# Optimization experiments

Hardware: AMD Instinct MI355X
Metric: run time of the kernel (lower is better)

Reference implementation:

```python
import jax, jax.numpy as jnp
import numpy as np

N = 1_048_576   # sampled points
E = 32          # grid feature dim (static_grid.out_dim / xyzt_grid.out_dim)
H = 64          # hidden_dim
GEO = 15        # geo_feat_dim
V = 3           # input_ch_views


def setup_inputs() -> dict:
    key = jax.random.key(0)
    ks = jax.random.split(key, 32)
    rn = lambda k, s: jax.random.normal(k, s, jnp.float32)
    w = lambda k, i, o: rn(k, (i, o)) * (1.0 / np.sqrt(i))
    inp = {
        'embedded_xyz': rn(ks[0], (N, E)),
        'embedded_xyzt': rn(ks[1], (N, E)),
        'embedded_xyzt_cam': rn(ks[2], (N, E)),
        'input_views': rn(ks[3], (N, V)),
        'keep_mask_bg': (jax.random.uniform(ks[4], (N,)) < 0.95).astype(jnp.float32),
        'keep_mask_fg': (jax.random.uniform(ks[5], (N,)) < 0.95).astype(jnp.float32),
        'keep_mask_actor': (jax.random.uniform(ks[6], (N,)) < 0.95).astype(jnp.float32),
    }
    # sigma nets: E->H, H->H, H->(1+1+GEO); color nets: in->H, H->H, H->H, H->3
    sigma_shapes = [(E, H), (H, H), (H, 1 + 1 + GEO)]
    bg_color_shapes = [(V + GEO, H), (H, H), (H, H), (H, 3)]      # BG uses viewdirs
    dyn_color_shapes = [(GEO, H), (H, H), (H, H), (H, 3)]          # use_viewdirs_FG=False
    ki = 7
    for pref, cshapes in (('bg', bg_color_shapes), ('fg', dyn_color_shapes), ('actor', dyn_color_shapes)):
        for l, (i, o) in enumerate(sigma_shapes):
            inp[f'{pref}_s{l}'] = w(ks[ki], i, o); ki += 1
        for l, (i, o) in enumerate(cshapes):
            inp[f'{pref}_c{l}'] = w(ks[ki], i, o); ki += 1
    return inp


def _mlp(h, Ws):
    # bias-free Linear + ReLU chain, no ReLU after last layer
    for W in Ws[:-1]:
        h = jax.nn.relu(h @ W)
    return h @ Ws[-1]


def _branch(emb, views, sW, cW, mask):
    h = _mlp(emb, sW)                       # [N, 1+1+GEO]
    sigma = jax.nn.softplus(h[:, 0]) * mask # relu_act = Softplus
    geo = h[:, 2:]
    ci = geo if views is None else jnp.concatenate([views, geo], axis=-1)
    color = jax.nn.sigmoid(_mlp(ci, cW)) * mask[:, None]
    return sigma, color


def reference(embedded_xyz, embedded_xyzt, embedded_xyzt_cam, input_views,
              keep_mask_bg, keep_mask_fg, keep_mask_actor,
              bg_s0, bg_s1, bg_s2, bg_c0, bg_c1, bg_c2, bg_c3,
              fg_s0, fg_s1, fg_s2, fg_c0, fg_c1, fg_c2, fg_c3,
              actor_s0, actor_s1, actor_s2, actor_c0, actor_c1, actor_c2, actor_c3):
    bg_sigma, bg_color = _branch(embedded_xyz, input_views,
                                 [bg_s0, bg_s1, bg_s2], [bg_c0, bg_c1, bg_c2, bg_c3], keep_mask_bg)
    fg_sigma, fg_color = _branch(embedded_xyzt, None,
                                 [fg_s0, fg_s1, fg_s2], [fg_c0, fg_c1, fg_c2, fg_c3], keep_mask_fg)
    ac_sigma, ac_color = _branch(embedded_xyzt_cam, None,
                                 [actor_s0, actor_s1, actor_s2], [actor_c0, actor_c1, actor_c2, actor_c3], keep_mask_actor)
    sigma = bg_sigma + fg_sigma + ac_sigma + 1e-9
    color = ((bg_sigma / sigma)[:, None] * bg_color
             + (fg_sigma / sigma)[:, None] * fg_color
             + (ac_sigma / sigma)[:, None] * ac_color)
    return jnp.concatenate([color, sigma[:, None]], axis=-1)  # [N, 4]
```

## Files before the change

### kernel.cpp

```cpp
#include <hip/hip_runtime.h>

typedef unsigned int  uint;
typedef unsigned short ushort;

#define N_PTS  1048576
#define BLOCK  1024
#define WAVES  16
#define NPT    4
#define CHUNK  (WAVES * NPT * 16)
#define NCHUNK (N_PTS / CHUNK)
#define GRID   256

static_assert(N_PTS % CHUNK == 0, "chunking");
static_assert(NCHUNK % GRID == 0, "grid stride");

typedef __attribute__((ext_vector_type(8))) _Float16 f16x8;
typedef __attribute__((ext_vector_type(2))) _Float16 f16x2;
typedef __attribute__((ext_vector_type(4))) float    f32x4;

struct Params {
    const float* emb[3];
    const float* views;
    const float* mask[3];
    const float* w[21];
    float* out;
};

__device__ uint g_wbuf[3 * 9216];

#define OFF_S0 0
#define OFF_S1 2048
#define OFF_S2 6144
#define OFF_C0 7168
#define OFF_C1 9216
#define OFF_C2 13312
#define OFF_C3 17408
#define BR_SZ  18432

__device__ __forceinline__ uint cvt2w(float a, float b) {
    f16x2 v = {(_Float16)a, (_Float16)b};
    return __builtin_bit_cast(uint, v);
}
__device__ __forceinline__ uint cvt2(float a, float b) {
    return __builtin_bit_cast(uint, __builtin_amdgcn_cvt_pkrtz(a, b));
}
__device__ __forceinline__ uint maxz(uint x) {
    f16x2 v = __builtin_bit_cast(f16x2, x);
    f16x2 z = {(_Float16)0.f, (_Float16)0.f};
    return __builtin_bit_cast(uint, __builtin_elementwise_max(v, z));
}

__device__ __forceinline__ f32x4 MFMA(f16x8 a, f16x8 b, f32x4 c) {
    return __builtin_amdgcn_mfma_f32_16x16x32_f16(a, b, c, 0, 0, 0);
}

__device__ __forceinline__ float fast_rcp(float x) { return __builtin_amdgcn_rcpf(x); }

__device__ __forceinline__ float wphys(int L, int br, const float* W, int kp, int m) {
    if (L == 0) return W[kp * 64 + m];
    const int g = (kp & 31) >> 3, e = kp & 7, h = kp >> 5;
    if (L == 3) {
        if (e < 4) {
            const int f = 4 * g + e;
            if (f < 1) return 0.f;
            return (br == 0) ? W[(f + 2) * 64 + m] : W[(f - 1) * 64 + m];
        }
        return (br == 0 && g == 0 && e <= 6) ? W[(e - 4) * 64 + m] : 0.f;
    }
    const int f = 16 * ((e >> 2) + 2 * h) + 4 * g + (e & 3);
    if (L == 2) return W[f * 17 + (m == 0 ? 0 : m + 1)];
    if (L == 6) return (m < 3) ? W[f * 3 + m] : 0.f;
    return W[f * 64 + m];
}

__global__ void prep_weights(Params P) {
    const int idx = blockIdx.x * 256 + threadIdx.x;
    const int br  = idx / 9216;
    const int rem = idx - br * 9216;
    int L, q;
    if      (rem < 1024) { L = 0; q = rem;        }
    else if (rem < 3072) { L = 1; q = rem - 1024; }
    else if (rem < 3584) { L = 2; q = rem - 3072; }
    else if (rem < 4608) { L = 3; q = rem - 3584; }
    else if (rem < 6656) { L = 4; q = rem - 4608; }
    else if (rem < 8704) { L = 5; q = rem - 6656; }
    else                 { L = 6; q = rem - 8704; }
    const float* W   = P.w[br * 7 + L];
    const int kk_n   = (L == 0 || L == 3) ? 1 : 2;
    const int E  = q * 2;
    const int b  = E >> 9;
    const int ln = (E >> 3) & 63;
    const int e  = E & 7;
    const int mt = b / kk_n;
    const int kk = b - mt * kk_n;
    const int m  = mt * 16 + (ln & 15);
    const int kp = kk * 32 + (ln >> 4) * 8 + e;
    g_wbuf[idx] = cvt2w(wphys(L, br, W, kp, m), wphys(L, br, W, kp + 1, m));
}

template<bool RELU>
__device__ __forceinline__ void handoff64(const f32x4 (&a)[4], uint4 &b0, uint4 &b1) {
#pragma unroll
    for (int h = 0; h < 2; ++h) {
        const f32x4 &lo = a[2 * h], &hi = a[2 * h + 1];
        uint w0 = cvt2(lo[0], lo[1]);
        uint w1 = cvt2(lo[2], lo[3]);
        uint w2 = cvt2(hi[0], hi[1]);
        uint w3 = cvt2(hi[2], hi[3]);
        if (RELU) { w0 = maxz(w0); w1 = maxz(w1); w2 = maxz(w2); w3 = maxz(w3); }
        uint4 &b = h ? b1 : b0;
        b.x = w0; b.y = w1; b.z = w2; b.w = w3;
    }
}

__device__ __forceinline__ void layer64(const ushort* lw, int lane,
                                        uint4 (&b0)[NPT], uint4 (&b1)[NPT]) {
    f16x8 wf[8];
#pragma unroll
    for (int b = 0; b < 8; ++b) wf[b] = *(const f16x8*)(lw + b * 512 + lane * 8);
#pragma unroll
    for (int t = 0; t < NPT; ++t) {
        const f16x8 i0 = __builtin_bit_cast(f16x8, b0[t]);
        const f16x8 i1 = __builtin_bit_cast(f16x8, b1[t]);
        f32x4 acc[4];
#pragma unroll
        for (int mt = 0; mt < 4; ++mt) {
            f32x4 a = (f32x4){0.f, 0.f, 0.f, 0.f};
            a = MFMA(wf[mt * 2 + 0], i0, a);
            a = MFMA(wf[mt * 2 + 1], i1, a);
            acc[mt] = a;
        }
        handoff64<true>(acc, b0[t], b1[t]);
    }
}

__global__ __launch_bounds__(BLOCK, 4) void nerf_main(Params P) {
    __shared__ __align__(16) ushort lds_w[3 * BR_SZ];

    const int tid = threadIdx.x;
    {
        const uint4* src = (const uint4*)g_wbuf;
        uint4* dst = (uint4*)lds_w;
        for (int i = tid; i < 6912; i += BLOCK) dst[i] = src[i];
    }
    __syncthreads();

    const int wave = tid >> 6;
    const int lane = tid & 63;
    const int c = lane & 15;
    const int g = lane >> 4;

#pragma unroll 1
    for (int ch = blockIdx.x; ch < NCHUNK; ch += gridDim.x) {
        const int p0 = ch * CHUNK + wave * (NPT * 16);

        float stot[NPT], car[NPT], cag[NPT], cab[NPT];
#pragma unroll
        for (int t = 0; t < NPT; ++t) { stot[t] = 0.f; car[t] = 0.f; cag[t] = 0.f; cab[t] = 0.f; }

#pragma unroll 1
        for (int br = 0; br < 3; ++br) {
            const ushort* lw  = lds_w + br * BR_SZ;
            const float* emb  = P.emb[br];
            const float* msk  = P.mask[br];
            float sig_pre[NPT], rp[NPT], gp[NPT], bp[NPT];
            uint4 b0[NPT], b1[NPT];

            {
                f16x8 wf[4];
#pragma unroll
                for (int b = 0; b < 4; ++b)
                    wf[b] = *(const f16x8*)(lw + OFF_S0 + b * 512 + lane * 8);
#pragma unroll
                for (int t = 0; t < NPT; ++t) {
                    const float* ep = emb + (size_t)(p0 + t * 16 + c) * 32 + g * 8;
                    const float4 ea = *(const float4*)ep;
                    const float4 eb = *(const float4*)(ep + 4);
                    uint4 iv;
                    iv.x = cvt2(ea.x, ea.y); iv.y = cvt2(ea.z, ea.w);
                    iv.z = cvt2(eb.x, eb.y); iv.w = cvt2(eb.z, eb.w);
                    const f16x8 inf = __builtin_bit_cast(f16x8, iv);
                    f32x4 acc[4];
#pragma unroll
                    for (int mt = 0; mt < 4; ++mt) {
                        f32x4 a = (f32x4){0.f, 0.f, 0.f, 0.f};
                        acc[mt] = MFMA(wf[mt], inf, a);
                    }
                    handoff64<true>(acc, b0[t], b1[t]);
                }
            }

            layer64(lw + OFF_S1, lane, b0, b1);

            {
                const f16x8 w0 = *(const f16x8*)(lw + OFF_S2 + 0 * 512 + lane * 8);
                const f16x8 w1 = *(const f16x8*)(lw + OFF_S2 + 1 * 512 + lane * 8);
#pragma unroll
                for (int t = 0; t < NPT; ++t) {
                    f32x4 a = (f32x4){0.f, 0.f, 0.f, 0.f};
                    a = MFMA(w0, __builtin_bit_cast(f16x8, b0[t]), a);
                    a = MFMA(w1, __builtin_bit_cast(f16x8, b1[t]), a);
                    sig_pre[t] = a[0];
                    uint4 nb;
                    nb.x = cvt2(a[0], a[1]);
                    nb.y = cvt2(a[2], a[3]);
                    nb.z = 0u; nb.w = 0u;
                    if (br == 0 && g == 0) {
                        const float* vp = P.views + (size_t)(p0 + t * 16 + c) * 3;
                        nb.z = cvt2(vp[0], vp[1]);
                        nb.w = cvt2(vp[2], 0.f);
                    }
                    b0[t] = nb;
                }
            }

            {
                f16x8 wf[4];
#pragma unroll
                for (int b = 0; b < 4; ++b)
                    wf[b] = *(const f16x8*)(lw + OFF_C0 + b * 512 + lane * 8);
#pragma unroll
                for (int t = 0; t < NPT; ++t) {
                    const f16x8 inf = __builtin_bit_cast(f16x8, b0[t]);
                    f32x4 acc[4];
#pragma unroll
                    for (int mt = 0; mt < 4; ++mt) {
                        f32x4 a = (f32x4){0.f, 0.f, 0.f, 0.f};
                        acc[mt] = MFMA(wf[mt], inf, a);
                    }
                    handoff64<true>(acc, b0[t], b1[t]);
                }
            }

            layer64(lw + OFF_C1, lane, b0, b1);
            layer64(lw + OFF_C2, lane, b0, b1);

            {
                const f16x8 w0 = *(const f16x8*)(lw + OFF_C3 + 0 * 512 + lane * 8);
                const f16x8 w1 = *(const f16x8*)(lw + OFF_C3 + 1 * 512 + lane * 8);
#pragma unroll
                for (int t = 0; t < NPT; ++t) {
                    f32x4 a = (f32x4){0.f, 0.f, 0.f, 0.f};
                    a = MFMA(w0, __builtin_bit_cast(f16x8, b0[t]), a);
                    a = MFMA(w1, __builtin_bit_cast(f16x8, b1[t]), a);
                    rp[t] = a[0]; gp[t] = a[1]; bp[t] = a[2];
                }
            }

#pragma unroll
            for (int t = 0; t < NPT; ++t) {
                const float mk = msk[p0 + t * 16 + c];
                const float x  = sig_pre[t];
                const float ex = __expf(x);
                const float sp = (x > 15.f) ? x : 0.69314718f * __log2f(1.f + ex);
                const float sb = sp * mk;
                stot[t] += sb;
                const float sm = sb * mk;
                car[t] += sm * fast_rcp(1.f + __expf(-rp[t]));
                cag[t] += sm * fast_rcp(1.f + __expf(-gp[t]));
                cab[t] += sm * fast_rcp(1.f + __expf(-bp[t]));
            }
        }

#pragma unroll
        for (int t = 0; t < NPT; ++t) {
            if (lane < 16) {
                const float s   = stot[t] + 1e-9f;
                const float inv = fast_rcp(s);
                float4 o;
                o.x = car[t] * inv; o.y = cag[t] * inv; o.z = cab[t] * inv; o.w = s;
                *(float4*)(P.out + (size_t)(p0 + t * 16 + lane) * 4) = o;
            }
        }
    }
}

extern "C" void kernel_launch(void* const* d_in, const int* in_sizes, int n_in,
                              void* d_out, int out_size, void* d_ws, size_t ws_size,
                              hipStream_t stream) {
    (void)in_sizes; (void)n_in; (void)d_ws; (void)ws_size; (void)out_size;
    Params P;
    P.emb[0] = (const float*)d_in[0];
    P.emb[1] = (const float*)d_in[1];
    P.emb[2] = (const float*)d_in[2];
    P.views  = (const float*)d_in[3];
    P.mask[0] = (const float*)d_in[4];
    P.mask[1] = (const float*)d_in[5];
    P.mask[2] = (const float*)d_in[6];
    for (int i = 0; i < 21; ++i) P.w[i] = (const float*)d_in[7 + i];
    P.out = (float*)d_out;
    prep_weights<<<108, 256, 0, stream>>>(P);
    nerf_main<<<GRID, BLOCK, 0, stream>>>(P);
}
```

Before: 138.6 us.

## Split fused three-branch kernel into per-branch kernels plus finalize pass

Replaces the single kernel that evaluates all three MLP branches per point with three templated per-branch kernels that accumulate weighted color and sigma into the output buffer, followed by a normalization kernel. Each kernel holds only one branch's weights in LDS and uses smaller blocks with fewer points per wave, aiming for more occupancy or more grid parallelism. In exchange it adds extra global read-modify-write traffic on the output buffer (about 16 MB per pass) plus three more kernel launches.

```diff
diff --git a/kernel.cpp b/kernel.cpp
--- a/kernel.cpp
+++ b/kernel.cpp
@@ -4,12 +4,12 @@
 typedef unsigned short ushort;
 
 #define N_PTS  1048576
-#define BLOCK  1024
-#define WAVES  16
-#define NPT    4
+#define BLOCK  512
+#define WAVES  8
+#define NPT    2
 #define CHUNK  (WAVES * NPT * 16)
 #define NCHUNK (N_PTS / CHUNK)
-#define GRID   256
+#define GRID   1024
 
 static_assert(N_PTS % CHUNK == 0, "chunking");
 static_assert(NCHUNK % GRID == 0, "grid stride");
@@ -134,145 +134,148 @@
     }
 }
 
-__global__ __launch_bounds__(BLOCK, 4) void nerf_main(Params P) {
-    __shared__ __align__(16) ushort lds_w[3 * BR_SZ];
+template<int BR>
+__global__ __launch_bounds__(BLOCK, 4) void nerf_branch(Params P) {
+    __shared__ __align__(16) ushort lds_w[BR_SZ];
 
     const int tid = threadIdx.x;
     {
-        const uint4* src = (const uint4*)g_wbuf;
+        const uint4* src = (const uint4*)(g_wbuf + BR * 9216);
         uint4* dst = (uint4*)lds_w;
-        for (int i = tid; i < 6912; i += BLOCK) dst[i] = src[i];
+        for (int i = tid; i < 2304; i += BLOCK) dst[i] = src[i];
     }
     __syncthreads();
 
-    const int wave = tid >> 6;
     const int lane = tid & 63;
     const int c = lane & 15;
     const int g = lane >> 4;
+    const float* emb = P.emb[BR];
+    const float* msk = P.mask[BR];
 
 #pragma unroll 1
     for (int ch = blockIdx.x; ch < NCHUNK; ch += gridDim.x) {
-        const int p0 = ch * CHUNK + wave * (NPT * 16);
-
-        float stot[NPT], car[NPT], cag[NPT], cab[NPT];
-#pragma unroll
-        for (int t = 0; t < NPT; ++t) { stot[t] = 0.f; car[t] = 0.f; cag[t] = 0.f; cab[t] = 0.f; }
-
-#pragma unroll 1
-        for (int br = 0; br < 3; ++br) {
-            const ushort* lw  = lds_w + br * BR_SZ;
-            const float* emb  = P.emb[br];
-            const float* msk  = P.mask[br];
-            float sig_pre[NPT], rp[NPT], gp[NPT], bp[NPT];
-            uint4 b0[NPT], b1[NPT];
-
-            {
-                f16x8 wf[4];
-#pragma unroll
-                for (int b = 0; b < 4; ++b)
-                    wf[b] = *(const f16x8*)(lw + OFF_S0 + b * 512 + lane * 8);
-#pragma unroll
-                for (int t = 0; t < NPT; ++t) {
-                    const float* ep = emb + (size_t)(p0 + t * 16 + c) * 32 + g * 8;
-                    const float4 ea = *(const float4*)ep;
-                    const float4 eb = *(const float4*)(ep + 4);
-                    uint4 iv;
-                    iv.x = cvt2(ea.x, ea.y); iv.y = cvt2(ea.z, ea.w);
-                    iv.z = cvt2(eb.x, eb.y); iv.w = cvt2(eb.z, eb.w);
-                    const f16x8 inf = __builtin_bit_cast(f16x8, iv);
-                    f32x4 acc[4];
-#pragma unroll
-                    for (int mt = 0; mt < 4; ++mt) {
-                        f32x4 a = (f32x4){0.f, 0.f, 0.f, 0.f};
-                        acc[mt] = MFMA(wf[mt], inf, a);
-                    }
-                    handoff64<true>(acc, b0[t], b1[t]);
+        const int p0 = ch * CHUNK + (tid >> 6) * (NPT * 16);
+
+        float sig_pre[NPT], rp[NPT], gp[NPT], bp[NPT];
+        uint4 b0[NPT], b1[NPT];
+
+        {
+            f16x8 wf[4];
+#pragma unroll
+            for (int b = 0; b < 4; ++b)
+                wf[b] = *(const f16x8*)(lds_w + OFF_S0 + b * 512 + lane * 8);
+#pragma unroll
+            for (int t = 0; t < NPT; ++t) {
+                const float* ep = emb + (size_t)(p0 + t * 16 + c) * 32 + g * 8;
+                const float4 ea = *(const float4*)ep;
+                const float4 eb = *(const float4*)(ep + 4);
+                uint4 iv;
+                iv.x = cvt2(ea.x, ea.y); iv.y = cvt2(ea.z, ea.w);
+                iv.z = cvt2(eb.x, eb.y); iv.w = cvt2(eb.z, eb.w);
+                const f16x8 inf = __builtin_bit_cast(f16x8, iv);
+                f32x4 acc[4];
+#pragma unroll
+                for (int mt = 0; mt < 4; ++mt) {
+                    f32x4 a = (f32x4){0.f, 0.f, 0.f, 0.f};
+                    acc[mt] = MFMA(wf[mt], inf, a);
                 }
-            }
-
-            layer64(lw + OFF_S1, lane, b0, b1);
-
-            {
-                const f16x8 w0 = *(const f16x8*)(lw + OFF_S2 + 0 * 512 + lane * 8);
-                const f16x8 w1 = *(const f16x8*)(lw + OFF_S2 + 1 * 512 + lane * 8);
-#pragma unroll
-                for (int t = 0; t < NPT; ++t) {
+                handoff64<true>(acc, b0[t], b1[t]);
+            }
+        }
+
+        layer64(lds_w + OFF_S1, lane, b0, b1);
+
+        {
+            const f16x8 w0 = *(const f16x8*)(lds_w + OFF_S2 + 0 * 512 + lane * 8);
+            const f16x8 w1 = *(const f16x8*)(lds_w + OFF_S2 + 1 * 512 + lane * 8);
+#pragma unroll
+            for (int t = 0; t < NPT; ++t) {
+                f32x4 a = (f32x4){0.f, 0.f, 0.f, 0.f};
+                a = MFMA(w0, __builtin_bit_cast(f16x8, b0[t]), a);
+                a = MFMA(w1, __builtin_bit_cast(f16x8, b1[t]), a);
+                sig_pre[t] = a[0];
+                uint4 nb;
+                nb.x = cvt2(a[0], a[1]);
+                nb.y = cvt2(a[2], a[3]);
+                nb.z = 0u; nb.w = 0u;
+                if (BR == 0 && g == 0) {
+                    const float* vp = P.views + (size_t)(p0 + t * 16 + c) * 3;
+                    nb.z = cvt2(vp[0], vp[1]);
+                    nb.w = cvt2(vp[2], 0.f);
+                }
+                b0[t] = nb;
+            }
+        }
+
+        {
+            f16x8 wf[4];
+#pragma unroll
+            for (int b = 0; b < 4; ++b)
+                wf[b] = *(const f16x8*)(lds_w + OFF_C0 + b * 512 + lane * 8);
+#pragma unroll
+            for (int t = 0; t < NPT; ++t) {
+                const f16x8 inf = __builtin_bit_cast(f16x8, b0[t]);
+                f32x4 acc[4];
+#pragma unroll
+                for (int mt = 0; mt < 4; ++mt) {
                     f32x4 a = (f32x4){0.f, 0.f, 0.f, 0.f};
-                    a = MFMA(w0, __builtin_bit_cast(f16x8, b0[t]), a);
-                    a = MFMA(w1, __builtin_bit_cast(f16x8, b1[t]), a);
-                    sig_pre[t] = a[0];
-                    uint4 nb;
-                    nb.x = cvt2(a[0], a[1]);
-                    nb.y = cvt2(a[2], a[3]);
-                    nb.z = 0u; nb.w = 0u;
-                    if (br == 0 && g == 0) {
-                        const float* vp = P.views + (size_t)(p0 + t * 16 + c) * 3;
-                        nb.z = cvt2(vp[0], vp[1]);
-                        nb.w = cvt2(vp[2], 0.f);
-                    }
-                    b0[t] = nb;
+                    acc[mt] = MFMA(wf[mt], inf, a);
                 }
-            }
-
-            {
-                f16x8 wf[4];
-#pragma unroll
-                for (int b = 0; b < 4; ++b)
-                    wf[b] = *(const f16x8*)(lw + OFF_C0 + b * 512 + lane * 8);
-#pragma unroll
-                for (int t = 0; t < NPT; ++t) {
-                    const f16x8 inf = __builtin_bit_cast(f16x8, b0[t]);
-                    f32x4 acc[4];
-#pragma unroll
-                    for (int mt = 0; mt < 4; ++mt) {
-                        f32x4 a = (f32x4){0.f, 0.f, 0.f, 0.f};
-                        acc[mt] = MFMA(wf[mt], inf, a);
-                    }
-                    handoff64<true>(acc, b0[t], b1[t]);
+                handoff64<true>(acc, b0[t], b1[t]);
+            }
+        }
+
+        layer64(lds_w + OFF_C1, lane, b0, b1);
+        layer64(lds_w + OFF_C2, lane, b0, b1);
+
+        {
+            const f16x8 w0 = *(const f16x8*)(lds_w + OFF_C3 + 0 * 512 + lane * 8);
+            const f16x8 w1 = *(const f16x8*)(lds_w + OFF_C3 + 1 * 512 + lane * 8);
+#pragma unroll
+            for (int t = 0; t < NPT; ++t) {
+                f32x4 a = (f32x4){0.f, 0.f, 0.f, 0.f};
+                a = MFMA(w0, __builtin_bit_cast(f16x8, b0[t]), a);
+                a = MFMA(w1, __builtin_bit_cast(f16x8, b1[t]), a);
+                rp[t] = a[0]; gp[t] = a[1]; bp[t] = a[2];
+            }
+        }
+
+#pragma unroll
+        for (int t = 0; t < NPT; ++t) {
+            const int pt = p0 + t * 16 + c;
+            const float mk = msk[pt];
+            const float x  = sig_pre[t];
+            const float ex = __expf(x);
+            const float sp = (x > 15.f) ? x : 0.69314718f * __log2f(1.f + ex);
+            const float sb = sp * mk;
+            const float sm = sb * mk;
+            const float car = sm * fast_rcp(1.f + __expf(-rp[t]));
+            const float cag = sm * fast_rcp(1.f + __expf(-gp[t]));
+            const float cab = sm * fast_rcp(1.f + __expf(-bp[t]));
+            if (lane < 16) {
+                float4* op = (float4*)(P.out + (size_t)pt * 4);
+                float4 o;
+                if (BR == 0) {
+                    o.x = car; o.y = cag; o.z = cab; o.w = sb;
+                } else {
+                    float4 prev = *op;
+                    o.x = prev.x + car; o.y = prev.y + cag;
+                    o.z = prev.z + cab; o.w = prev.w + sb;
                 }
-            }
-
-            layer64(lw + OFF_C1, lane, b0, b1);
-            layer64(lw + OFF_C2, lane, b0, b1);
-
-            {
-                const f16x8 w0 = *(const f16x8*)(lw + OFF_C3 + 0 * 512 + lane * 8);
-                const f16x8 w1 = *(const f16x8*)(lw + OFF_C3 + 1 * 512 + lane * 8);
-#pragma unroll
-                for (int t = 0; t < NPT; ++t) {
-                    f32x4 a = (f32x4){0.f, 0.f, 0.f, 0.f};
-                    a = MFMA(w0, __builtin_bit_cast(f16x8, b0[t]), a);
-                    a = MFMA(w1, __builtin_bit_cast(f16x8, b1[t]), a);
-                    rp[t] = a[0]; gp[t] = a[1]; bp[t] = a[2];
-                }
-            }
-
-#pragma unroll
-            for (int t = 0; t < NPT; ++t) {
-                const float mk = msk[p0 + t * 16 + c];
-                const float x  = sig_pre[t];
-                const float ex = __expf(x);
-                const float sp = (x > 15.f) ? x : 0.69314718f * __log2f(1.f + ex);
-                const float sb = sp * mk;
-                stot[t] += sb;
-                const float sm = sb * mk;
-                car[t] += sm * fast_rcp(1.f + __expf(-rp[t]));
-                cag[t] += sm * fast_rcp(1.f + __expf(-gp[t]));
-                cab[t] += sm * fast_rcp(1.f + __expf(-bp[t]));
-            }
-        }
-
-#pragma unroll
-        for (int t = 0; t < NPT; ++t) {
-            if (lane < 16) {
-                const float s   = stot[t] + 1e-9f;
-                const float inv = fast_rcp(s);
-                float4 o;
-                o.x = car[t] * inv; o.y = cag[t] * inv; o.z = cab[t] * inv; o.w = s;
-                *(float4*)(P.out + (size_t)(p0 + t * 16 + lane) * 4) = o;
-            }
-        }
-    }
+                *op = o;
+            }
+        }
+    }
+}
+
+__global__ __launch_bounds__(512) void nerf_finalize(float* out) {
+    const size_t pt = (size_t)blockIdx.x * 512 + threadIdx.x;
+    float4* op = (float4*)(out + pt * 4);
+    float4 o = *op;
+    const float s   = o.w + 1e-9f;
+    const float inv = fast_rcp(s);
+    o.x *= inv; o.y *= inv; o.z *= inv; o.w = s;
+    *op = o;
 }
 
 extern "C" void kernel_launch(void* const* d_in, const int* in_sizes, int n_in,
@@ -290,5 +293,8 @@
     for (int i = 0; i < 21; ++i) P.w[i] = (const float*)d_in[7 + i];
     P.out = (float*)d_out;
     prep_weights<<<108, 256, 0, stream>>>(P);
-    nerf_main<<<GRID, BLOCK, 0, stream>>>(P);
-}
+    nerf_branch<0><<<GRID, BLOCK, 0, stream>>>(P);
+    nerf_branch<1><<<GRID, BLOCK, 0, stream>>>(P);
+    nerf_branch<2><<<GRID, BLOCK, 0, stream>>>(P);
+    nerf_finalize<<<N_PTS / 512, 512, 0, stream>>>(P.out);
+}
```

Result: slower. 515.0 us (+271.4%).

## Halve points per wave and keep only 64x64 layer weights in LDS

Applied to the files above, without the earlier changes.

Shrinks the LDS weight buffer to hold only the three H×H layers per branch, repacked contiguously. The smaller first and last layers (S0, S2, C0, C3) are now read straight from the global weight buffer through the cache. NPT drops from 4 to 2, which cuts register pressure and LDS footprint so more waves can stay resident. The cost is more global loads for the small weights and more chunk iterations, each doing less work per weight-fragment load.

```diff
diff --git a/kernel.cpp b/kernel.cpp
--- a/kernel.cpp
+++ b/kernel.cpp
@@ -6,7 +6,7 @@
 #define N_PTS  1048576
 #define BLOCK  1024
 #define WAVES  16
-#define NPT    4
+#define NPT    2
 #define CHUNK  (WAVES * NPT * 16)
 #define NCHUNK (N_PTS / CHUNK)
 #define GRID   256
@@ -35,7 +35,11 @@
 #define OFF_C1 9216
 #define OFF_C2 13312
 #define OFF_C3 17408
-#define BR_SZ  18432
+
+#define LPB 12288
+#define LS1 0
+#define LC1 4096
+#define LC2 8192
 
 __device__ __forceinline__ uint cvt2w(float a, float b) {
     f16x2 v = {(_Float16)a, (_Float16)b};
@@ -135,24 +139,28 @@
 }
 
 __global__ __launch_bounds__(BLOCK, 4) void nerf_main(Params P) {
-    __shared__ __align__(16) ushort lds_w[3 * BR_SZ];
+    __shared__ __align__(16) ushort lds_w[3 * LPB];
 
     const int tid = threadIdx.x;
     {
-        const uint4* src = (const uint4*)g_wbuf;
+        const uint4* src4 = (const uint4*)g_wbuf;
         uint4* dst = (uint4*)lds_w;
-        for (int i = tid; i < 6912; i += BLOCK) dst[i] = src[i];
+        for (int i = tid; i < 4608; i += BLOCK) {
+            const int b = i / 1536, r = i - b * 1536;
+            const int seg = r >> 9, off = r & 511;
+            const int sbase = (seg == 0) ? 256 : (seg == 1) ? 1152 : 1664;
+            dst[i] = src4[b * 2304 + sbase + off];
+        }
     }
     __syncthreads();
 
-    const int wave = tid >> 6;
     const int lane = tid & 63;
     const int c = lane & 15;
     const int g = lane >> 4;
 
 #pragma unroll 1
     for (int ch = blockIdx.x; ch < NCHUNK; ch += gridDim.x) {
-        const int p0 = ch * CHUNK + wave * (NPT * 16);
+        const int p0 = ch * CHUNK + (tid >> 6) * (NPT * 16);
 
         float stot[NPT], car[NPT], cag[NPT], cab[NPT];
 #pragma unroll
@@ -160,7 +168,8 @@
 
 #pragma unroll 1
         for (int br = 0; br < 3; ++br) {
-            const ushort* lw  = lds_w + br * BR_SZ;
+            const ushort* lw  = lds_w + br * LPB;
+            const ushort* gw  = (const ushort*)(g_wbuf + br * 9216);
             const float* emb  = P.emb[br];
             const float* msk  = P.mask[br];
             float sig_pre[NPT], rp[NPT], gp[NPT], bp[NPT];
@@ -170,7 +179,7 @@
                 f16x8 wf[4];
 #pragma unroll
                 for (int b = 0; b < 4; ++b)
-                    wf[b] = *(const f16x8*)(lw + OFF_S0 + b * 512 + lane * 8);
+                    wf[b] = *(const f16x8*)(gw + OFF_S0 + b * 512 + lane * 8);
 #pragma unroll
                 for (int t = 0; t < NPT; ++t) {
                     const float* ep = emb + (size_t)(p0 + t * 16 + c) * 32 + g * 8;
@@ -190,11 +199,11 @@
                 }
             }
 
-            layer64(lw + OFF_S1, lane, b0, b1);
+            layer64(lw + LS1, lane, b0, b1);
 
             {
-                const f16x8 w0 = *(const f16x8*)(lw + OFF_S2 + 0 * 512 + lane * 8);
-                const f16x8 w1 = *(const f16x8*)(lw + OFF_S2 + 1 * 512 + lane * 8);
+                const f16x8 w0 = *(const f16x8*)(gw + OFF_S2 + 0 * 512 + lane * 8);
+                const f16x8 w1 = *(const f16x8*)(gw + OFF_S2 + 1 * 512 + lane * 8);
 #pragma unroll
                 for (int t = 0; t < NPT; ++t) {
                     f32x4 a = (f32x4){0.f, 0.f, 0.f, 0.f};
@@ -218,7 +227,7 @@
                 f16x8 wf[4];
 #pragma unroll
                 for (int b = 0; b < 4; ++b)
-                    wf[b] = *(const f16x8*)(lw + OFF_C0 + b * 512 + lane * 8);
+                    wf[b] = *(const f16x8*)(gw + OFF_C0 + b * 512 + lane * 8);
 #pragma unroll
                 for (int t = 0; t < NPT; ++t) {
                     const f16x8 inf = __builtin_bit_cast(f16x8, b0[t]);
@@ -232,12 +241,12 @@
                 }
             }
 
-            layer64(lw + OFF_C1, lane, b0, b1);
-            layer64(lw + OFF_C2, lane, b0, b1);
+            layer64(lw + LC1, lane, b0, b1);
+            layer64(lw + LC2, lane, b0, b1);
 
             {
-                const f16x8 w0 = *(const f16x8*)(lw + OFF_C3 + 0 * 512 + lane * 8);
-                const f16x8 w1 = *(const f16x8*)(lw + OFF_C3 + 1 * 512 + lane * 8);
+                const f16x8 w0 = *(const f16x8*)(gw + OFF_C3 + 0 * 512 + lane * 8);
+                const f16x8 w1 = *(const f16x8*)(gw + OFF_C3 + 1 * 512 + lane * 8);
 #pragma unroll
                 for (int t = 0; t < NPT; ++t) {
                     f32x4 a = (f32x4){0.f, 0.f, 0.f, 0.f};
```

Result: slower. 151.7 us (+9.4%).
